# Optimization experiments

Measured on AMD Instinct MI355X. Metric: run time of the kernel, lower is better.

Reference implementation:

```python
import jax, jax.numpy as jnp
import numpy as np

B, T, C, H = 2, 2048, 2048, 16
D = C // H  # head_dim = 128
SCALE = 1.0 / np.sqrt(D)


def setup_inputs() -> dict:
    key = jax.random.key(0)
    ks = jax.random.split(key, 9)
    x = jax.random.normal(ks[0], (B, T, C), dtype=jnp.float32)
    # additive causal mask [T, T]
    attn_mask = jnp.where(jnp.tril(jnp.ones((T, T), dtype=bool)), 0.0, -1e9).astype(jnp.float32)
    s_cc = 1.0 / np.sqrt(C)
    s_cd = 1.0 / np.sqrt(C)
    Wq = jax.random.normal(ks[1], (C, C), dtype=jnp.float32) * s_cc
    Wk = jax.random.normal(ks[2], (D, C), dtype=jnp.float32) * s_cd
    Wv = jax.random.normal(ks[3], (D, C), dtype=jnp.float32) * s_cd
    Wo = jax.random.normal(ks[4], (C, C), dtype=jnp.float32) * s_cc
    bq = jnp.zeros((C,), jnp.float32)
    bk = jnp.zeros((D,), jnp.float32)
    bv = jnp.zeros((D,), jnp.float32)
    bo = jnp.zeros((C,), jnp.float32)
    return {"x": x, "attn_mask": attn_mask, "Wq": Wq, "bq": bq, "Wk": Wk,
            "bk": bk, "Wv": Wv, "bv": bv, "Wo": Wo, "bo": bo}


def reference(x, attn_mask, Wq, bq, Wk, bk, Wv, bv, Wo, bo):
    # projections (torch Linear: x @ W.T + b)
    q = (x @ Wq.T + bq).reshape(B, T, H, D).transpose(0, 2, 1, 3)  # [B,H,T,D]
    k = x @ Wk.T + bk                                              # [B,T,D] single KV head
    v = x @ Wv.T + bv                                              # [B,T,D]
    # scores: broadcast shared K over all H query heads
    scores = jnp.einsum('bhtd,bsd->bhts', q, k) * SCALE            # [B,H,T,T]
    scores = scores + attn_mask  # [T,T] broadcasts over B,H
    attn = jax.nn.softmax(scores, axis=-1)
    out = jnp.einsum('bhts,bsd->bhtd', attn, v)                    # [B,H,T,D]
    out = out.transpose(0, 2, 1, 3).reshape(B, T, C)
    return out @ Wo.T + bo
```

## Files before the change

kernel.cpp:

```cpp
#include <hip/hip_runtime.h>
#include <stdint.h>

typedef unsigned short u16;
typedef __attribute__((ext_vector_type(8))) __bf16 bf16x8;
typedef __attribute__((ext_vector_type(4))) __bf16 bf16x4;
typedef __attribute__((ext_vector_type(4))) float f32x4;
typedef __attribute__((ext_vector_type(8))) u16 u16x8;
typedef __attribute__((ext_vector_type(4))) short s16x4;
typedef __attribute__((ext_vector_type(2))) unsigned int u32x2;

#define B_SZ 2
#define T_SZ 2048
#define C_SZ 2048
#define H_SZ 16
#define D_SZ 128
#define NQKV 2304
#define ATT_SCALE 0.08838834764831845f
#define LOG2E_SCALE 0.12751744f
#define DEFER_THR 90.50967f

typedef __attribute__((address_space(1))) void* as1_void_p;
typedef __attribute__((address_space(3))) void* as3_void_p;

__device__ __forceinline__ u16 f2b(float f) {
  union { float f; uint32_t u; } c; c.f = f;
  return (u16)((c.u + 0x7FFFu + ((c.u >> 16) & 1u)) >> 16);
}

__device__ __forceinline__ void gload_lds16(const u16* g, u16* l) {
  __builtin_amdgcn_global_load_lds((as1_void_p)g, (as3_void_p)l, 16, 0, 0);
}

__device__ __forceinline__ f32x4 mfma16(s16x4 a, s16x4 b, f32x4 c) {
#if __has_builtin(__builtin_amdgcn_mfma_f32_16x16x16bf16_1k)
  return __builtin_amdgcn_mfma_f32_16x16x16bf16_1k(a, b, c, 0, 0, 0);
#elif __has_builtin(__builtin_amdgcn_mfma_f32_16x16x16_bf16)
  return __builtin_amdgcn_mfma_f32_16x16x16_bf16(
      __builtin_bit_cast(bf16x4, a), __builtin_bit_cast(bf16x4, b), c, 0, 0, 0);
#else
  u32x2 ua = __builtin_bit_cast(u32x2, a);
  u32x2 ub = __builtin_bit_cast(u32x2, b);
  asm("s_nop 1\n\tv_mfma_f32_16x16x16_bf16 %0, %1, %2, %0\n\ts_nop 7"
      : "+v"(c) : "v"(ua), "v"(ub));
  return c;
#endif
}

__device__ __forceinline__ void cast4(const float* __restrict__ in,
                                      u16* __restrict__ out, int lb, int tid) {
  int idx = lb * 1024 + tid * 4;
  float4 f = *(const float4*)&in[idx];
  ushort4 o4;
  o4.x = f2b(f.x); o4.y = f2b(f.y); o4.z = f2b(f.z); o4.w = f2b(f.w);
  *(ushort4*)&out[idx] = o4;
}

__global__ __launch_bounds__(256) void prep(const float* __restrict__ x,
                                            const float* __restrict__ Wq,
                                            const float* __restrict__ Wk,
                                            const float* __restrict__ Wv,
                                            const float* __restrict__ Wo,
                                            const float* __restrict__ bq,
                                            const float* __restrict__ bk,
                                            const float* __restrict__ bv,
                                            u16* __restrict__ xb,
                                            u16* __restrict__ wqkv,
                                            u16* __restrict__ wob,
                                            float* __restrict__ bqkv) {
  const int bid = blockIdx.x, tid = threadIdx.x;
  if (bid < 8192)       cast4(x,  xb,              bid,         tid);
  else if (bid < 12288) cast4(Wq, wqkv,            bid - 8192,  tid);
  else if (bid < 12544) cast4(Wk, wqkv + 4194304,  bid - 12288, tid);
  else if (bid < 12800) cast4(Wv, wqkv + 4456448,  bid - 12544, tid);
  else if (bid < 16896) cast4(Wo, wob,             bid - 12800, tid);
  else {
    int e = (bid - 16896) * 1024 + tid * 4;
#pragma unroll
    for (int j = 0; j < 4; j++) {
      int i = e + j;
      if (i < NQKV)
        bqkv[i] = i < C_SZ ? bq[i] : (i < C_SZ + D_SZ ? bk[i - C_SZ] : bv[i - C_SZ - D_SZ]);
    }
  }
}

template <typename OutT>
__global__ __launch_bounds__(256) void gemm_bt(const u16* __restrict__ A,
                                               const u16* __restrict__ Bm,
                                               const float* __restrict__ bias,
                                               OutT* __restrict__ C,
                                               int K, int ldc) {
  __shared__ u16 lsA[2][128 * 32];
  __shared__ u16 lsB[2][128 * 32];
  const int tid = threadIdx.x;
  const int lane = tid & 63;
  const int wave = tid >> 6;
  const int wr = wave >> 1, wc = wave & 1;
  const int l16 = lane & 15, lq = lane >> 4;
  const int nwg = gridDim.x * gridDim.y;
  int wg = blockIdx.y * gridDim.x + blockIdx.x;
  wg = (wg & 7) * (nwg >> 3) + (wg >> 3);
  const int brow = (wg / gridDim.x) * 128;
  const int bcol = (wg % gridDim.x) * 128;

  f32x4 acc[4][4] = {};

  auto STAGE = [&](int k0, int bs) {
#pragma unroll
    for (int i = 0; i < 2; i++) {
      const int woff = (i * 4 + wave) * 512;
      const int eoff = woff + lane * 8;
      const int r = eoff >> 5, c = eoff & 31;
      gload_lds16(A + (size_t)(brow + r) * K + k0 + c, &lsA[bs][woff]);
      gload_lds16(Bm + (size_t)(bcol + r) * K + k0 + c, &lsB[bs][woff]);
    }
  };

  STAGE(0, 0);
  __syncthreads();
  int cur = 0;
  for (int k0 = 0; k0 < K; k0 += 32) {
    if (k0 + 32 < K) STAGE(k0 + 32, cur ^ 1);

    bf16x8 af[4], bfr[4];
#pragma unroll
    for (int mi = 0; mi < 4; mi++)
      af[mi] = *(const bf16x8*)&lsA[cur][(wr * 64 + mi * 16 + l16) * 32 + lq * 8];
#pragma unroll
    for (int ni = 0; ni < 4; ni++)
      bfr[ni] = *(const bf16x8*)&lsB[cur][(wc * 64 + ni * 16 + l16) * 32 + lq * 8];
#pragma unroll
    for (int mi = 0; mi < 4; mi++)
#pragma unroll
      for (int ni = 0; ni < 4; ni++)
        acc[mi][ni] = __builtin_amdgcn_mfma_f32_16x16x32_bf16(af[mi], bfr[ni], acc[mi][ni], 0, 0, 0);

    __syncthreads();
    cur ^= 1;
  }

#pragma unroll
  for (int mi = 0; mi < 4; mi++)
#pragma unroll
    for (int ni = 0; ni < 4; ni++) {
      const int col = bcol + wc * 64 + ni * 16 + l16;
      const float bb = bias ? bias[col] : 0.0f;
#pragma unroll
      for (int r = 0; r < 4; r++) {
        const int row = brow + wr * 64 + mi * 16 + lq * 4 + r;
        const float v = acc[mi][ni][r] + bb;
        if constexpr (sizeof(OutT) == 2) {
          ((u16*)C)[(size_t)row * ldc + col] = f2b(v);
        } else {
          ((float*)C)[(size_t)row * ldc + col] = v;
        }
      }
    }
}

__global__ __launch_bounds__(256) void transpose_v(const u16* __restrict__ qkv,
                                                   u16* __restrict__ vT) {
  __shared__ u16 tile[64 * 136];
  const int tid = threadIdx.x;
  const int t0 = blockIdx.x * 64;
  const int b = blockIdx.y;
#pragma unroll
  for (int i = 0; i < 4; i++) {
    int idx = (i * 256 + tid) * 8;
    int r = idx >> 7, c = idx & 127;
    u16x8 v = *(const u16x8*)&qkv[(size_t)(b * T_SZ + t0 + r) * NQKV + (C_SZ + D_SZ) + c];
    *(u16x8*)&tile[r * 136 + c] = v;
  }
  __syncthreads();
#pragma unroll
  for (int i = 0; i < 4; i++) {
    int idx = (i * 256 + tid) * 8;
    int d = idx >> 6, t = idx & 63;
    u16x8 v;
#pragma unroll
    for (int j = 0; j < 8; j++) v[j] = tile[(t + j) * 136 + d];
    *(u16x8*)&vT[(size_t)(b * D_SZ + d) * T_SZ + t0 + t] = v;
  }
}

__device__ __forceinline__ void qk_part(const u16* lk, const bf16x8 (&aq)[4],
                                        f32x4 (&s)[4], int l16, int lq) {
#pragma unroll
  for (int kk = 0; kk < 4; kk++) {
#pragma unroll
    for (int nb = 0; nb < 4; nb++) {
      const int row = nb * 16 + l16;
      const bf16x8 kf = *(const bf16x8*)&lk[row * 128 + (((kk * 4 + lq) ^ (row & 7)) << 3)];
      s[nb] = __builtin_amdgcn_mfma_f32_16x16x32_bf16(kf, aq[kk], s[nb], 0, 0, 0);
    }
  }
}

template <bool DIAG>
__device__ __forceinline__ void sm_pv(const u16* lv, f32x4 (&s)[4], f32x4 (&o)[8],
                                      float& lp, float& m, int q_rel, int l16, int lq) {
  if (DIAG) {
#pragma unroll
    for (int nb = 0; nb < 4; nb++)
#pragma unroll
      for (int rr = 0; rr < 4; rr++)
        if (nb * 16 + lq * 4 + rr > q_rel) s[nb][rr] -= 1e9f;
  }
  float m0 = fmaxf(fmaxf(s[0][0], s[0][1]), fmaxf(s[0][2], s[0][3]));
  float m1 = fmaxf(fmaxf(s[1][0], s[1][1]), fmaxf(s[1][2], s[1][3]));
  float m2 = fmaxf(fmaxf(s[2][0], s[2][1]), fmaxf(s[2][2], s[2][3]));
  float m3 = fmaxf(fmaxf(s[3][0], s[3][1]), fmaxf(s[3][2], s[3][3]));
  float mx = fmaxf(fmaxf(m0, m1), fmaxf(m2, m3));
  if (__any(mx > m + DEFER_THR)) {
    float rmx = fmaxf(mx, __shfl_xor(mx, 16, 64));
    rmx = fmaxf(rmx, __shfl_xor(rmx, 32, 64));
    const float mnew = fmaxf(m, rmx);
    const float alpha = exp2f((m - mnew) * LOG2E_SCALE);
    m = mnew;
    lp *= alpha;
#pragma unroll
    for (int nd = 0; nd < 8; nd++)
#pragma unroll
      for (int e = 0; e < 4; e++) o[nd][e] *= alpha;
  }
#pragma unroll
  for (int nb = 0; nb < 4; nb++) {
    bf16x4 pbv;
#pragma unroll
    for (int e = 0; e < 4; e++) {
      const float p = exp2f((s[nb][e] - m) * LOG2E_SCALE);
      lp += p;
      pbv[e] = (__bf16)p;
    }
    const s16x4 pb = __builtin_bit_cast(s16x4, pbv);
    __builtin_amdgcn_s_setprio(1);
#pragma unroll
    for (int nd = 0; nd < 8; nd++) {
      const int row = nd * 16 + l16;
      const s16x4 av = *(const s16x4*)&lv[row * 64 +
          ((((nb << 1) | (lq >> 1)) ^ (row & 7)) << 3) + ((lq & 1) << 2)];
      o[nd] = mfma16(av, pb, o[nd]);
    }
    __builtin_amdgcn_s_setprio(0);
  }
}

__global__ __launch_bounds__(512, 4) void attn_fwd(const u16* __restrict__ qkv,
                                                   const u16* __restrict__ vT,
                                                   u16* __restrict__ out) {
  __shared__ u16 lsK[2][64 * 128];
  __shared__ u16 lsV[2][128 * 64];
  const int tid = threadIdx.x;
  const int wv = tid >> 6, lane = tid & 63;
  const int l16 = lane & 15, lq = lane >> 4;
  const int h = blockIdx.y;
  const int b = blockIdx.z;
  const int qH = (b == 0) ? (31 - blockIdx.x) : (16 + blockIdx.x);
  const int qL = 31 - qH;
  const int bT = b * T_SZ;
  const int qt = (wv < 4) ? qH : qL;
  const int wq0 = qt * 64 + (wv & 3) * 16;

  bf16x8 aq[4];
  {
    const size_t qrow = (size_t)(bT + wq0 + l16) * NQKV + h * D_SZ;
#pragma unroll
    for (int kk = 0; kk < 4; kk++)
      aq[kk] = *(const bf16x8*)&qkv[qrow + kk * 32 + lq * 8];
  }

  f32x4 o[8] = {};
  float lp = 0.f, m = -INFINITY;

  const u16 *kp0, *kp1, *vp0, *vp1;
  {
    const int kr0 = tid >> 4,         kc0 = tid & 15;
    const int kr1 = (512 + tid) >> 4, kc1 = tid & 15;
    kp0 = qkv + (size_t)(bT + kr0) * NQKV + C_SZ + (size_t)((kc0 ^ (kr0 & 7)) * 8);
    kp1 = qkv + (size_t)(bT + kr1) * NQKV + C_SZ + (size_t)((kc1 ^ (kr1 & 7)) * 8);
    const int vr0 = tid >> 3,         vc0 = tid & 7;
    const int vr1 = (512 + tid) >> 3, vc1 = tid & 7;
    vp0 = vT + (size_t)(b * D_SZ + vr0) * T_SZ + (vc0 ^ (vr0 & 7)) * 8;
    vp1 = vT + (size_t)(b * D_SZ + vr1) * T_SZ + (vc1 ^ (vr1 & 7)) * 8;
  }
  const int kd0 = wv * 512, kd1 = (8 + wv) * 512;

  auto STAGE_K = [&](int kt, int bf) {
    const size_t off = (size_t)kt * (64 * NQKV);
    gload_lds16(kp0 + off, &lsK[bf][kd0]);
    gload_lds16(kp1 + off, &lsK[bf][kd1]);
  };
  auto STAGE_V = [&](int kt, int bf) {
    const int off = kt * 64;
    gload_lds16(vp0 + off, &lsV[bf][kd0]);
    gload_lds16(vp1 + off, &lsV[bf][kd1]);
  };

  const int nkt = qH + 1;
  STAGE_K(0, 0);
  STAGE_V(0, 0);
  __syncthreads();
  int cur = 0;
  for (int kt = 0; kt < nkt; kt++) {
    if (kt + 1 < nkt) {
      STAGE_K(kt + 1, cur ^ 1);
      STAGE_V(kt + 1, cur ^ 1);
    }
    if (kt <= qt) {
      f32x4 s[4] = {};
      __builtin_amdgcn_s_setprio(1);
      qk_part(lsK[cur], aq, s, l16, lq);
      __builtin_amdgcn_s_setprio(0);
      if (kt < qt)
        sm_pv<false>(lsV[cur], s, o, lp, m, 0, l16, lq);
      else
        sm_pv<true>(lsV[cur], s, o, lp, m, wq0 + l16 - kt * 64, l16, lq);
    }
    asm volatile("s_waitcnt vmcnt(0)" ::: "memory");
    __builtin_amdgcn_sched_barrier(0);
    __builtin_amdgcn_s_barrier();
    cur ^= 1;
  }

  lp += __shfl_xor(lp, 16, 64);
  lp += __shfl_xor(lp, 32, 64);
  const float r = __builtin_amdgcn_rcpf(lp);
  const size_t rowb = (size_t)(bT + wq0 + l16) * C_SZ + h * D_SZ;
#pragma unroll
  for (int nd = 0; nd < 8; nd++) {
    ushort4 sv;
    sv.x = f2b(o[nd][0] * r); sv.y = f2b(o[nd][1] * r);
    sv.z = f2b(o[nd][2] * r); sv.w = f2b(o[nd][3] * r);
    *(ushort4*)&out[rowb + nd * 16 + lq * 4] = sv;
  }
}

extern "C" void kernel_launch(void* const* d_in, const int* in_sizes, int n_in,
                              void* d_out, int out_size, void* d_ws, size_t ws_size,
                              hipStream_t stream) {
  const float* x  = (const float*)d_in[0];
  const float* Wq = (const float*)d_in[2];
  const float* bq = (const float*)d_in[3];
  const float* Wk = (const float*)d_in[4];
  const float* bk = (const float*)d_in[5];
  const float* Wv = (const float*)d_in[6];
  const float* bv = (const float*)d_in[7];
  const float* Wo = (const float*)d_in[8];
  const float* bo = (const float*)d_in[9];
  float* out = (float*)d_out;

  char* ws = (char*)d_ws;
  if (ws_size < 71312384) return;
  u16* xb     = (u16*)(ws + 0);
  u16* wqkv   = (u16*)(ws + 16777216);
  u16* wob    = (u16*)(ws + 26214400);
  u16* qkv    = (u16*)(ws + 34603008);
  u16* vT     = (u16*)(ws + 53477376);
  u16* ao     = (u16*)(ws + 54525952);
  float* bqkv = (float*)(ws + 71303168);

  prep<<<16899, 256, 0, stream>>>(x, Wq, Wk, Wv, Wo, bq, bk, bv, xb, wqkv, wob, bqkv);

  gemm_bt<u16><<<dim3(18, 32), 256, 0, stream>>>(xb, wqkv, bqkv, qkv, 2048, NQKV);
  transpose_v<<<dim3(32, 2), 256, 0, stream>>>(qkv, vT);
  attn_fwd<<<dim3(16, 16, 2), 512, 0, stream>>>(qkv, vT, ao);
  gemm_bt<float><<<dim3(16, 32), 256, 0, stream>>>(ao, wob, bo, out, 2048, 2048);
}
```

Measured before the change: 205.0 us.

## Software-pipeline QK ahead of softmax-PV and widen GEMM K-tile with LDS swizzle

The attention loop now computes the next tile's QK scores while doing softmax and PV for the current tile. K is staged two tiles ahead and V one tile ahead, with ping-pong score registers, so the MFMA work of QK can overlap the softmax. The projection GEMM moves from a K step of 32 to 64, with an XOR swizzle in LDS to avoid bank conflicts and half as many barriers. The cost is more registers for the extra score buffer and double the GEMM LDS footprint, which may lower occupancy.

```diff
diff --git a/kernel.cpp b/kernel.cpp
--- a/kernel.cpp
+++ b/kernel.cpp
@@ -90,8 +90,8 @@
                                                const float* __restrict__ bias,
                                                OutT* __restrict__ C,
                                                int K, int ldc) {
-  __shared__ u16 lsA[2][128 * 32];
-  __shared__ u16 lsB[2][128 * 32];
+  __shared__ u16 lsA[2][128 * 64];
+  __shared__ u16 lsB[2][128 * 64];
   const int tid = threadIdx.x;
   const int lane = tid & 63;
   const int wave = tid >> 6;
@@ -107,33 +107,41 @@
 
   auto STAGE = [&](int k0, int bs) {
 #pragma unroll
-    for (int i = 0; i < 2; i++) {
+    for (int i = 0; i < 4; i++) {
+      const int idx = (i * 4 + wave) * 64 + lane;
+      const int r = idx >> 3, cd = idx & 7;
+      const int sc = (cd ^ (r & 7)) << 3;
       const int woff = (i * 4 + wave) * 512;
-      const int eoff = woff + lane * 8;
-      const int r = eoff >> 5, c = eoff & 31;
-      gload_lds16(A + (size_t)(brow + r) * K + k0 + c, &lsA[bs][woff]);
-      gload_lds16(Bm + (size_t)(bcol + r) * K + k0 + c, &lsB[bs][woff]);
+      gload_lds16(A + (size_t)(brow + r) * K + k0 + sc, &lsA[bs][woff]);
+      gload_lds16(Bm + (size_t)(bcol + r) * K + k0 + sc, &lsB[bs][woff]);
     }
   };
 
   STAGE(0, 0);
   __syncthreads();
   int cur = 0;
-  for (int k0 = 0; k0 < K; k0 += 32) {
-    if (k0 + 32 < K) STAGE(k0 + 32, cur ^ 1);
-
-    bf16x8 af[4], bfr[4];
-#pragma unroll
-    for (int mi = 0; mi < 4; mi++)
-      af[mi] = *(const bf16x8*)&lsA[cur][(wr * 64 + mi * 16 + l16) * 32 + lq * 8];
-#pragma unroll
-    for (int ni = 0; ni < 4; ni++)
-      bfr[ni] = *(const bf16x8*)&lsB[cur][(wc * 64 + ni * 16 + l16) * 32 + lq * 8];
-#pragma unroll
-    for (int mi = 0; mi < 4; mi++)
-#pragma unroll
-      for (int ni = 0; ni < 4; ni++)
-        acc[mi][ni] = __builtin_amdgcn_mfma_f32_16x16x32_bf16(af[mi], bfr[ni], acc[mi][ni], 0, 0, 0);
+  for (int k0 = 0; k0 < K; k0 += 64) {
+    if (k0 + 64 < K) STAGE(k0 + 64, cur ^ 1);
+
+#pragma unroll
+    for (int kk = 0; kk < 2; kk++) {
+      bf16x8 af[4], bfr[4];
+#pragma unroll
+      for (int mi = 0; mi < 4; mi++) {
+        const int r = wr * 64 + mi * 16 + l16;
+        af[mi] = *(const bf16x8*)&lsA[cur][r * 64 + (((kk * 4 + lq) ^ (r & 7)) << 3)];
+      }
+#pragma unroll
+      for (int ni = 0; ni < 4; ni++) {
+        const int r = wc * 64 + ni * 16 + l16;
+        bfr[ni] = *(const bf16x8*)&lsB[cur][r * 64 + (((kk * 4 + lq) ^ (r & 7)) << 3)];
+      }
+#pragma unroll
+      for (int mi = 0; mi < 4; mi++)
+#pragma unroll
+        for (int ni = 0; ni < 4; ni++)
+          acc[mi][ni] = __builtin_amdgcn_mfma_f32_16x16x32_bf16(af[mi], bfr[ni], acc[mi][ni], 0, 0, 0);
+    }
 
     __syncthreads();
     cur ^= 1;
@@ -297,29 +305,44 @@
   };
 
   const int nkt = qH + 1;
+
+  f32x4 sA[4] = {}, sB[4] = {};
+
+  auto ITER = [&](int t, f32x4 (&scur)[4], f32x4 (&snext)[4]) {
+    if (t + 1 < nkt) STAGE_V(t + 1, (t + 1) & 1);
+    if (t + 2 < nkt) STAGE_K(t + 2, t & 1);
+#pragma unroll
+    for (int nb = 0; nb < 4; nb++) snext[nb] = f32x4{0.f, 0.f, 0.f, 0.f};
+    if (t + 1 <= qt) {
+      __builtin_amdgcn_s_setprio(1);
+      qk_part(lsK[(t + 1) & 1], aq, snext, l16, lq);
+      __builtin_amdgcn_s_setprio(0);
+    }
+    if (t <= qt) {
+      if (t < qt) sm_pv<false>(lsV[t & 1], scur, o, lp, m, 0, l16, lq);
+      else        sm_pv<true >(lsV[t & 1], scur, o, lp, m, wq0 + l16 - t * 64, l16, lq);
+    }
+    asm volatile("s_waitcnt vmcnt(0)" ::: "memory");
+    __builtin_amdgcn_sched_barrier(0);
+    __builtin_amdgcn_s_barrier();
+  };
+
   STAGE_K(0, 0);
   STAGE_V(0, 0);
   __syncthreads();
-  int cur = 0;
-  for (int kt = 0; kt < nkt; kt++) {
-    if (kt + 1 < nkt) {
-      STAGE_K(kt + 1, cur ^ 1);
-      STAGE_V(kt + 1, cur ^ 1);
-    }
-    if (kt <= qt) {
-      f32x4 s[4] = {};
-      __builtin_amdgcn_s_setprio(1);
-      qk_part(lsK[cur], aq, s, l16, lq);
-      __builtin_amdgcn_s_setprio(0);
-      if (kt < qt)
-        sm_pv<false>(lsV[cur], s, o, lp, m, 0, l16, lq);
-      else
-        sm_pv<true>(lsV[cur], s, o, lp, m, wq0 + l16 - kt * 64, l16, lq);
-    }
-    asm volatile("s_waitcnt vmcnt(0)" ::: "memory");
-    __builtin_amdgcn_sched_barrier(0);
-    __builtin_amdgcn_s_barrier();
-    cur ^= 1;
+  qk_part(lsK[0], aq, sA, l16, lq);
+  STAGE_K(1, 1);
+  asm volatile("s_waitcnt vmcnt(0)" ::: "memory");
+  __builtin_amdgcn_sched_barrier(0);
+  __builtin_amdgcn_s_barrier();
+
+  int kt = 0;
+  while (kt < nkt) {
+    ITER(kt, sA, sB);
+    kt++;
+    if (kt >= nkt) break;
+    ITER(kt, sB, sA);
+    kt++;
   }
 
   lp += __shfl_xor(lp, 16, 64);
```

After: 209.1 us. About the same (+2.0%).
